# Performance work log

Hardware: AMD Instinct MI355X
Metric: run time of the kernel (lower is better)

Reference implementation:

```python
import jax, jax.numpy as jnp
import numpy as np

B = 262144
IN = 12
HID = 256
OUT = 12


def setup_inputs() -> dict:
    key = jax.random.key(0)
    ks = jax.random.split(key, 7)
    def lin(k, fan_in, fan_out):
        kw, kb = jax.random.split(k)
        bound = 1.0 / np.sqrt(fan_in)
        W = jax.random.uniform(kw, (fan_in, fan_out), jnp.float32, -bound, bound)
        b = jax.random.uniform(kb, (fan_out,), jnp.float32, -bound, bound)
        return W, b
    W1, b1 = lin(ks[0], IN, HID)
    W2, b2 = lin(ks[1], HID, HID)
    W3, b3 = lin(ks[2], HID, OUT)
    inp = jax.random.normal(ks[3], (B, IN), jnp.float32)
    return {"inp": inp, "W1": W1, "b1": b1, "W2": W2, "b2": b2, "W3": W3, "b3": b3}


def _forward(inp, W1, b1, W2, b2, W3, b3):
    h = jax.nn.relu(inp @ W1 + b1)
    h = jax.nn.relu(h @ W2 + b2)
    x = h @ W3 + b3  # [B, 12]

    pos = jnp.tanh(x[:, 0:3])
    vel = jnp.tanh(x[:, 3:6])
    pts = jax.nn.sigmoid(x[:, 6:7])
    clus = jnp.tanh(x[:, 7:10])
    sun = jnp.tanh(x[:, 10:12])

    # position clipped to unit sphere
    dist = jnp.linalg.norm(pos, axis=1, keepdims=True)  # [B,1]
    pos_c = jnp.where(dist > 1.0, pos / dist, pos)

    # inspected points: over-estimates set to 1, under-estimates set to previous
    prev = inp[:, 6:7]
    pts_c = jnp.where(pts > 1.0, 1.0, pts)
    pts_c = jnp.where(pts < prev, prev, pts_c)

    # cluster: push away from deputy if moving toward it, then clip to unit sphere
    delta = clus - inp[:, 7:10]
    deputy = inp[:, 0:3] - inp[:, 7:10]
    nd = deputy / jnp.linalg.norm(deputy, axis=1, keepdims=True)
    dd = jnp.einsum('ij,ij->i', delta, deputy)[:, None]  # [B,1]
    offset = jnp.where(dd > 0.0, clus - nd, clus)
    cdist = jnp.linalg.norm(offset, axis=1, keepdims=True)
    # NOTE: non-exceeding rows keep the ORIGINAL tanh prediction (torch semantics)
    clus_c = jnp.where(cdist > 1.0, offset / cdist, clus)

    # sun angle projected onto unit circle
    sun_c = sun / jnp.linalg.norm(sun, axis=1, keepdims=True)

    return jnp.concatenate([pos_c, vel, pts_c, clus_c, sun_c], axis=1)


def reference(inp, W1, b1, W2, b2, W3, b3):
    return _forward(inp, W1, b1, W2, b2, W3, b3)
```

## Files before the change

kernel.cpp:

```cpp
#include <hip/hip_runtime.h>
#include <math.h>

#define NIN 12
#define HID 256
#define NOUT 12
#define BM 64
#define NBLK (262144 / BM)

typedef _Float16 f16;
typedef f16 f16x8 __attribute__((ext_vector_type(8)));
typedef float f32x4 __attribute__((ext_vector_type(4)));

__device__ __forceinline__ void gll16(const void* g, void* l) {
    __builtin_amdgcn_global_load_lds(
        (const __attribute__((address_space(1))) unsigned int*)g,
        (__attribute__((address_space(3))) unsigned int*)l, 16, 0, 0);
}

__global__ void prep_w2(const float* __restrict__ W2, f16* __restrict__ w2p) {
    const int e = (blockIdx.x * 256 + threadIdx.x) * 4;
    const int k = e >> 8, col0 = e & 255;
    const float4 w = *(const float4*)(W2 + k * HID + col0);
    const int s = k >> 5, lgw = (k >> 3) & 3, j = k & 7;
    #pragma unroll
    for (int q = 0; q < 4; ++q) {
        const float v = ((const float*)&w)[q];
        const f16 hi = (f16)v;
        const f16 lo = (f16)(v - (float)hi);
        const int c = col0 + q, ct = c >> 4, cc = c & 15, l = (lgw << 4) | cc;
        w2p[(size_t)(((s*2 + 0)*16 + ct)*64 + l)*8 + j] = hi;
        w2p[(size_t)(((s*2 + 1)*16 + ct)*64 + l)*8 + j] = lo;
    }
}

__global__ __launch_bounds__(256, 3)
void mlp_main(const float* __restrict__ inp, const float* __restrict__ W1,
              const float* __restrict__ b1, const float* __restrict__ W2,
              const float* __restrict__ b2, const float* __restrict__ W3,
              const float* __restrict__ b3, const f16* __restrict__ w2p,
              float* __restrict__ out)
{
    __shared__ __align__(16) unsigned char smem[48896];
    __shared__ int nflag;
    __shared__ int flaglist[16];

    f16*   Bl   = (f16*)smem;
    float* W3s  = (float*)(smem + 32768);
    float* b2s  = (float*)(smem + 45056);
    float* h1f  = (float*)(smem + 46080);
    float* h2f  = (float*)(smem + 47104);
    float* psum = (float*)(smem + 48128);

    const int t    = threadIdx.x;
    const int lane = t & 63;
    const int wid  = t >> 6;
    const int cl   = lane & 15;
    const int lg   = lane >> 4;
    const int row0 = blockIdx.x * BM;

    if (t == 0) nflag = 0;

    {
        const char* w3c = (const char*)W3;
        #pragma unroll
        for (int i = 0; i < 3; ++i) {
            const int off = (wid*3 + i) * 1024;
            gll16(w3c + off + lane*16, (char*)W3s + off);
        }
        if (wid == 0) gll16((const char*)b2 + lane*16, (char*)b2s);
    }

    const int myrow = row0 + wid*16 + cl;
    float xin[12];
    {
        const f32x4* ip = (const f32x4*)(inp + (size_t)myrow * NIN);
        const f32x4 a = ip[0], b = ip[1], c = ip[2];
        xin[0]=a.x; xin[1]=a.y; xin[2]=a.z; xin[3]=a.w;
        xin[4]=b.x; xin[5]=b.y; xin[6]=b.z; xin[7]=b.w;
        xin[8]=c.x; xin[9]=c.y; xin[10]=c.z; xin[11]=c.w;
    }

    f32x4 acc[16];
    {
        const f32x4 zero = {0.f, 0.f, 0.f, 0.f};
        #pragma unroll
        for (int ct = 0; ct < 16; ++ct) acc[ct] = zero;
    }
    for (int s = 0; s < 8; ++s) {
        __syncthreads();
        const char* src = (const char*)w2p + (size_t)s * 32768;
        #pragma unroll
        for (int i = 0; i < 8; ++i) {
            const int off = (i*4 + wid) * 1024;
            gll16(src + off + lane*16, (char*)Bl + off);
        }
        const int k0 = 32*s + 8*lg;
        float a0[8];
        {
            const f32x4 bb0 = *(const f32x4*)(b1 + k0);
            const f32x4 bb1 = *(const f32x4*)(b1 + k0 + 4);
            a0[0]=bb0.x; a0[1]=bb0.y; a0[2]=bb0.z; a0[3]=bb0.w;
            a0[4]=bb1.x; a0[5]=bb1.y; a0[6]=bb1.z; a0[7]=bb1.w;
        }
        #pragma unroll
        for (int m = 0; m < 12; ++m) {
            const float xm = xin[m];
            const f32x4 w0 = *(const f32x4*)(W1 + m*HID + k0);
            const f32x4 w1 = *(const f32x4*)(W1 + m*HID + k0 + 4);
            a0[0] = fmaf(xm, w0.x, a0[0]); a0[1] = fmaf(xm, w0.y, a0[1]);
            a0[2] = fmaf(xm, w0.z, a0[2]); a0[3] = fmaf(xm, w0.w, a0[3]);
            a0[4] = fmaf(xm, w1.x, a0[4]); a0[5] = fmaf(xm, w1.y, a0[5]);
            a0[6] = fmaf(xm, w1.z, a0[6]); a0[7] = fmaf(xm, w1.w, a0[7]);
        }
        f16x8 ahi, alo;
        #pragma unroll
        for (int j = 0; j < 8; ++j) {
            const float h = fmaxf(a0[j], 0.f);
            const f16 hi = (f16)h;
            ahi[j] = hi;
            alo[j] = (f16)(h - (float)hi);
        }
        asm volatile("s_waitcnt vmcnt(0)" ::: "memory");
        __syncthreads();
        #pragma unroll
        for (int ct = 0; ct < 16; ++ct) {
            const f16x8 bhi = *(const f16x8*)((const char*)Bl + (size_t)(( 0 + ct)*64 + lane)*16);
            const f16x8 blo = *(const f16x8*)((const char*)Bl + (size_t)((16 + ct)*64 + lane)*16);
            acc[ct] = __builtin_amdgcn_mfma_f32_16x16x32_f16(ahi, bhi, acc[ct], 0, 0, 0);
            acc[ct] = __builtin_amdgcn_mfma_f32_16x16x32_f16(ahi, blo, acc[ct], 0, 0, 0);
            acc[ct] = __builtin_amdgcn_mfma_f32_16x16x32_f16(alo, bhi, acc[ct], 0, 0, 0);
        }
    }

    float x[12];
    {
        float part[4][8];
        #pragma unroll
        for (int q = 0; q < 4; ++q)
            #pragma unroll
            for (int jj = 0; jj < 8; ++jj) part[q][jj] = 0.f;

        #pragma unroll
        for (int ct = 0; ct < 16; ++ct) {
            const int col = ct*16 + cl;
            const float bv = b2s[col];
            const f32x4 w3a = *(const f32x4*)(W3s + col*12);
            const f32x4 w3b = *(const f32x4*)(W3s + col*12 + 4);
            #pragma unroll
            for (int q = 0; q < 4; ++q) {
                const float h2 = fmaxf(acc[ct][q] + bv, 0.f);
                part[q][0] = fmaf(h2, w3a.x, part[q][0]);
                part[q][1] = fmaf(h2, w3a.y, part[q][1]);
                part[q][2] = fmaf(h2, w3a.z, part[q][2]);
                part[q][3] = fmaf(h2, w3a.w, part[q][3]);
                part[q][4] = fmaf(h2, w3b.x, part[q][4]);
                part[q][5] = fmaf(h2, w3b.y, part[q][5]);
                part[q][6] = fmaf(h2, w3b.z, part[q][6]);
                part[q][7] = fmaf(h2, w3b.w, part[q][7]);
            }
        }
        #pragma unroll
        for (int m = 1; m < 16; m <<= 1) {
            #pragma unroll
            for (int q = 0; q < 4; ++q)
                #pragma unroll
                for (int jj = 0; jj < 8; ++jj)
                    part[q][jj] += __shfl_xor(part[q][jj], m);
        }
        if (cl < 4) {
            #pragma unroll
            for (int jj = 0; jj < 8; ++jj) x[jj] = part[cl][jj];
        }
    }
    {
        float part[4][4];
        #pragma unroll
        for (int q = 0; q < 4; ++q)
            #pragma unroll
            for (int jj = 0; jj < 4; ++jj) part[q][jj] = 0.f;

        #pragma unroll
        for (int ct = 0; ct < 16; ++ct) {
            const int col = ct*16 + cl;
            const float bv = b2s[col];
            const f32x4 w3c = *(const f32x4*)(W3s + col*12 + 8);
            #pragma unroll
            for (int q = 0; q < 4; ++q) {
                const float h2 = fmaxf(acc[ct][q] + bv, 0.f);
                part[q][0] = fmaf(h2, w3c.x, part[q][0]);
                part[q][1] = fmaf(h2, w3c.y, part[q][1]);
                part[q][2] = fmaf(h2, w3c.z, part[q][2]);
                part[q][3] = fmaf(h2, w3c.w, part[q][3]);
            }
        }
        #pragma unroll
        for (int m = 1; m < 16; m <<= 1) {
            #pragma unroll
            for (int q = 0; q < 4; ++q)
                #pragma unroll
                for (int jj = 0; jj < 4; ++jj)
                    part[q][jj] += __shfl_xor(part[q][jj], m);
        }
        if (cl < 4) {
            #pragma unroll
            for (int jj = 0; jj < 4; ++jj) x[8 + jj] = part[cl][jj];
        }
    }

    if (cl < 4) {
        const int R = wid*16 + 4*lg + cl;
        const int grow = row0 + R;
        #pragma unroll
        for (int jj = 0; jj < 12; ++jj) x[jj] += b3[jj];

        const f32x4* ip = (const f32x4*)(inp + (size_t)grow * NIN);
        const f32x4 iA = ip[0], iB = ip[1], iC = ip[2];
        const float in0=iA.x, in1=iA.y, in2=iA.z, in6=iB.z, in7=iB.w, in8=iC.x, in9=iC.y;

        const float pos0=tanhf(x[0]), pos1=tanhf(x[1]), pos2=tanhf(x[2]);
        const float vel0=tanhf(x[3]), vel1=tanhf(x[4]), vel2=tanhf(x[5]);
        const float pts = 1.f/(1.f+expf(-x[6]));
        const float cl0=tanhf(x[7]), cl1=tanhf(x[8]), cl2=tanhf(x[9]);
        const float sn0=tanhf(x[10]), sn1=tanhf(x[11]);

        const float dist = sqrtf(pos0*pos0 + pos1*pos1 + pos2*pos2);
        float pc0=pos0, pc1=pos1, pc2=pos2;
        if (dist > 1.0f) { pc0 = pos0/dist; pc1 = pos1/dist; pc2 = pos2/dist; }

        const float prev = in6;
        float pts_c = (pts > 1.0f) ? 1.0f : pts;
        pts_c = (pts < prev) ? prev : pts_c;

        const float de0 = cl0-in7, de1 = cl1-in8, de2 = cl2-in9;
        const float dp0 = in0-in7, dp1 = in1-in8, dp2 = in2-in9;
        const float dpn = sqrtf(dp0*dp0 + dp1*dp1 + dp2*dp2);
        const float nd0 = dp0/dpn, nd1 = dp1/dpn, nd2 = dp2/dpn;
        const float dd  = de0*dp0 + de1*dp1 + de2*dp2;
        float off0, off1, off2;
        if (dd > 0.0f) { off0 = cl0-nd0; off1 = cl1-nd1; off2 = cl2-nd2; }
        else           { off0 = cl0;     off1 = cl1;     off2 = cl2;     }
        const float cdist = sqrtf(off0*off0 + off1*off1 + off2*off2);
        float cc0, cc1, cc2;
        if (cdist > 1.0f) { cc0 = off0/cdist; cc1 = off1/cdist; cc2 = off2/cdist; }
        else              { cc0 = cl0;        cc1 = cl1;        cc2 = cl2;        }

        const float snn = sqrtf(sn0*sn0 + sn1*sn1);
        const float sc0 = sn0/snn, sc1 = sn1/snn;

        if (fabsf(dd) < 2e-4f || (dd > 0.f && fabsf(cdist - 1.f) < 2e-4f)) {
            const int slot = atomicAdd(&nflag, 1);
            if (slot < 16) flaglist[slot] = R;
        }

        f32x4* dst = (f32x4*)(out + (size_t)grow * NOUT);
        f32x4 o0 = {pc0, pc1, pc2, vel0};
        f32x4 o1 = {vel1, vel2, pts_c, cc0};
        f32x4 o2 = {cc1, cc2, sc0, sc1};
        dst[0] = o0; dst[1] = o1; dst[2] = o2;
    }
    __syncthreads();

    const int nf = (nflag < 16) ? nflag : 16;
    for (int f = 0; f < nf; ++f) {
        const int grow = row0 + flaglist[f];
        {
            float a = b1[t];
            const float* xr = inp + (size_t)grow * NIN;
            #pragma unroll
            for (int m = 0; m < 12; ++m) a = fmaf(xr[m], W1[m*HID + t], a);
            h1f[t] = fmaxf(a, 0.f);
        }
        __syncthreads();
        {
            float a = b2[t];
            for (int k = 0; k < HID; ++k) a = fmaf(h1f[k], W2[k*HID + t], a);
            h2f[t] = fmaxf(a, 0.f);
        }
        __syncthreads();
        if (t < 12*16) {
            const int jj = t >> 4, seg = t & 15;
            float a = 0.f;
            #pragma unroll
            for (int u = 0; u < 16; ++u) a = fmaf(h2f[seg*16 + u], W3[(seg*16 + u)*NOUT + jj], a);
            psum[jj*16 + seg] = a;
        }
        __syncthreads();
        if (t == 0) {
            float xx[12];
            #pragma unroll
            for (int jj = 0; jj < 12; ++jj) {
                float sacc = b3[jj];
                for (int g = 0; g < 16; ++g) sacc += psum[jj*16 + g];
                xx[jj] = sacc;
            }
            const float* xr = inp + (size_t)grow * NIN;
            const float in0=xr[0], in1=xr[1], in2=xr[2], in6=xr[6], in7=xr[7], in8=xr[8], in9=xr[9];
            const float pos0=tanhf(xx[0]), pos1=tanhf(xx[1]), pos2=tanhf(xx[2]);
            const float vel0=tanhf(xx[3]), vel1=tanhf(xx[4]), vel2=tanhf(xx[5]);
            const float pts = 1.f/(1.f+expf(-xx[6]));
            const float cl0=tanhf(xx[7]), cl1=tanhf(xx[8]), cl2=tanhf(xx[9]);
            const float sn0=tanhf(xx[10]), sn1=tanhf(xx[11]);
            const float dist = sqrtf(pos0*pos0 + pos1*pos1 + pos2*pos2);
            float pc0=pos0, pc1=pos1, pc2=pos2;
            if (dist > 1.0f) { pc0 = pos0/dist; pc1 = pos1/dist; pc2 = pos2/dist; }
            const float prev = in6;
            float pts_c = (pts > 1.0f) ? 1.0f : pts;
            pts_c = (pts < prev) ? prev : pts_c;
            const float de0 = cl0-in7, de1 = cl1-in8, de2 = cl2-in9;
            const float dp0 = in0-in7, dp1 = in1-in8, dp2 = in2-in9;
            const float dpn = sqrtf(dp0*dp0 + dp1*dp1 + dp2*dp2);
            const float nd0 = dp0/dpn, nd1 = dp1/dpn, nd2 = dp2/dpn;
            const float dd  = de0*dp0 + de1*dp1 + de2*dp2;
            float off0, off1, off2;
            if (dd > 0.0f) { off0 = cl0-nd0; off1 = cl1-nd1; off2 = cl2-nd2; }
            else           { off0 = cl0;     off1 = cl1;     off2 = cl2;     }
            const float cdist = sqrtf(off0*off0 + off1*off1 + off2*off2);
            float cc0, cc1, cc2;
            if (cdist > 1.0f) { cc0 = off0/cdist; cc1 = off1/cdist; cc2 = off2/cdist; }
            else              { cc0 = cl0;        cc1 = cl1;        cc2 = cl2;        }
            const float snn = sqrtf(sn0*sn0 + sn1*sn1);
            const float sc0 = sn0/snn, sc1 = sn1/snn;
            float* dst = out + (size_t)grow * NOUT;
            dst[0]=pc0; dst[1]=pc1; dst[2]=pc2; dst[3]=vel0; dst[4]=vel1; dst[5]=vel2;
            dst[6]=pts_c; dst[7]=cc0; dst[8]=cc1; dst[9]=cc2; dst[10]=sc0; dst[11]=sc1;
        }
        __syncthreads();
    }
}

extern "C" void kernel_launch(void* const* d_in, const int* in_sizes, int n_in,
                              void* d_out, int out_size, void* d_ws, size_t ws_size,
                              hipStream_t stream) {
    const float* inp = (const float*)d_in[0];
    const float* W1  = (const float*)d_in[1];
    const float* b1  = (const float*)d_in[2];
    const float* W2  = (const float*)d_in[3];
    const float* b2  = (const float*)d_in[4];
    const float* W3  = (const float*)d_in[5];
    const float* b3  = (const float*)d_in[6];
    float* out = (float*)d_out;
    f16* w2p = (f16*)d_ws;

    hipLaunchKernelGGL(prep_w2, dim3(64), dim3(256), 0, stream, W2, w2p);
    hipLaunchKernelGGL(mlp_main, dim3(NBLK), dim3(256), 0, stream,
                       inp, W1, b1, W2, b2, W3, b3, (const f16*)w2p, out);
}
```

Baseline: 254.0 us.

## Double-buffer W2 slabs and split output columns across 8 waves

Raises the block to 512 threads. The 8 waves split the 256 hidden output columns in two halves, so each wave holds 8 accumulators instead of 16. W2 slabs are double-buffered in LDS and the next slab is prefetched while MFMAs run on the current one, which removes the sync-load-wait bubble at every k step. W3 is loaded after the loop into the freed buffer, and partial outputs from the two column halves are reduced through LDS before the epilogue. In exchange, LDS per block grows to about 71 KB, the layer-1 ReLU work is duplicated across the column halves, and an extra reduction sync is added.

```diff
diff --git a/kernel.cpp b/kernel.cpp
--- a/kernel.cpp
+++ b/kernel.cpp
@@ -5,6 +5,7 @@
 #define HID 256
 #define NOUT 12
 #define BM 64
+#define THREADS 512
 #define NBLK (262144 / BM)
 
 typedef _Float16 f16;
@@ -33,44 +34,43 @@
     }
 }
 
-__global__ __launch_bounds__(256, 3)
+__global__ __launch_bounds__(THREADS, 4)
 void mlp_main(const float* __restrict__ inp, const float* __restrict__ W1,
               const float* __restrict__ b1, const float* __restrict__ W2,
               const float* __restrict__ b2, const float* __restrict__ W3,
               const float* __restrict__ b3, const f16* __restrict__ w2p,
               float* __restrict__ out)
 {
-    __shared__ __align__(16) unsigned char smem[48896];
+    __shared__ __align__(16) unsigned char smem[72704];
     __shared__ int nflag;
     __shared__ int flaglist[16];
 
-    f16*   Bl   = (f16*)smem;
-    float* W3s  = (float*)(smem + 32768);
-    float* b2s  = (float*)(smem + 45056);
-    float* h1f  = (float*)(smem + 46080);
-    float* h2f  = (float*)(smem + 47104);
-    float* psum = (float*)(smem + 48128);
+    float* b2s  = (float*)(smem + 65536);
+    float* psum = (float*)(smem + 66560);
+    float* W3s  = (float*)smem;
+    float* h1f  = (float*)(smem + 12288);
+    float* h2f  = (float*)(smem + 13312);
 
     const int t    = threadIdx.x;
     const int lane = t & 63;
     const int wid  = t >> 6;
+    const int wr   = wid & 3;
+    const int wc   = wid >> 2;
     const int cl   = lane & 15;
     const int lg   = lane >> 4;
     const int row0 = blockIdx.x * BM;
 
     if (t == 0) nflag = 0;
 
-    {
-        const char* w3c = (const char*)W3;
-        #pragma unroll
-        for (int i = 0; i < 3; ++i) {
-            const int off = (wid*3 + i) * 1024;
-            gll16(w3c + off + lane*16, (char*)W3s + off);
-        }
-        if (wid == 0) gll16((const char*)b2 + lane*16, (char*)b2s);
-    }
-
-    const int myrow = row0 + wid*16 + cl;
+    if (t < 64) gll16((const char*)b2 + t*16, smem + 65536 + t*16);
+    {
+        const char* src = (const char*)w2p;
+        #pragma unroll
+        for (int i = 0; i < 4; ++i)
+            gll16(src + (i*THREADS + t)*16, smem + (i*THREADS + t)*16);
+    }
+
+    const int myrow = row0 + wr*16 + cl;
     float xin[12];
     {
         const f32x4* ip = (const f32x4*)(inp + (size_t)myrow * NIN);
@@ -80,20 +80,14 @@
         xin[8]=c.x; xin[9]=c.y; xin[10]=c.z; xin[11]=c.w;
     }
 
-    f32x4 acc[16];
+    f32x4 acc[8];
     {
         const f32x4 zero = {0.f, 0.f, 0.f, 0.f};
         #pragma unroll
-        for (int ct = 0; ct < 16; ++ct) acc[ct] = zero;
-    }
+        for (int ct = 0; ct < 8; ++ct) acc[ct] = zero;
+    }
+    #pragma unroll
     for (int s = 0; s < 8; ++s) {
-        __syncthreads();
-        const char* src = (const char*)w2p + (size_t)s * 32768;
-        #pragma unroll
-        for (int i = 0; i < 8; ++i) {
-            const int off = (i*4 + wid) * 1024;
-            gll16(src + off + lane*16, (char*)Bl + off);
-        }
         const int k0 = 32*s + 8*lg;
         float a0[8];
         {
@@ -120,18 +114,39 @@
             ahi[j] = hi;
             alo[j] = (f16)(h - (float)hi);
         }
+
         asm volatile("s_waitcnt vmcnt(0)" ::: "memory");
         __syncthreads();
-        #pragma unroll
-        for (int ct = 0; ct < 16; ++ct) {
-            const f16x8 bhi = *(const f16x8*)((const char*)Bl + (size_t)(( 0 + ct)*64 + lane)*16);
-            const f16x8 blo = *(const f16x8*)((const char*)Bl + (size_t)((16 + ct)*64 + lane)*16);
+
+        if (s < 7) {
+            const char* src = (const char*)w2p + (size_t)(s+1) * 32768;
+            char* dst = (char*)smem + ((s+1)&1) * 32768;
+            #pragma unroll
+            for (int i = 0; i < 4; ++i)
+                gll16(src + (i*THREADS + t)*16, dst + (i*THREADS + t)*16);
+        }
+
+        const char* bufr = (const char*)smem + (s&1) * 32768;
+        #pragma unroll
+        for (int ct = 0; ct < 8; ++ct) {
+            const int gct = wc*8 + ct;
+            const f16x8 bhi = *(const f16x8*)(bufr + (size_t)(( 0 + gct)*64 + lane)*16);
+            const f16x8 blo = *(const f16x8*)(bufr + (size_t)((16 + gct)*64 + lane)*16);
             acc[ct] = __builtin_amdgcn_mfma_f32_16x16x32_f16(ahi, bhi, acc[ct], 0, 0, 0);
             acc[ct] = __builtin_amdgcn_mfma_f32_16x16x32_f16(ahi, blo, acc[ct], 0, 0, 0);
             acc[ct] = __builtin_amdgcn_mfma_f32_16x16x32_f16(alo, bhi, acc[ct], 0, 0, 0);
         }
     }
 
+    __syncthreads();
+    {
+        const char* w3c = (const char*)W3;
+        gll16(w3c + t*16, smem + t*16);
+        if (t < 256) gll16(w3c + 8192 + t*16, smem + 8192 + t*16);
+    }
+    asm volatile("s_waitcnt vmcnt(0)" ::: "memory");
+    __syncthreads();
+
     float x[12];
     {
         float part[4][8];
@@ -141,8 +156,8 @@
             for (int jj = 0; jj < 8; ++jj) part[q][jj] = 0.f;
 
         #pragma unroll
-        for (int ct = 0; ct < 16; ++ct) {
-            const int col = ct*16 + cl;
+        for (int ct = 0; ct < 8; ++ct) {
+            const int col = (wc*8 + ct)*16 + cl;
             const float bv = b2s[col];
             const f32x4 w3a = *(const f32x4*)(W3s + col*12);
             const f32x4 w3b = *(const f32x4*)(W3s + col*12 + 4);
@@ -160,13 +175,12 @@
             }
         }
         #pragma unroll
-        for (int m = 1; m < 16; m <<= 1) {
+        for (int m = 1; m < 16; m <<= 1)
             #pragma unroll
             for (int q = 0; q < 4; ++q)
                 #pragma unroll
                 for (int jj = 0; jj < 8; ++jj)
                     part[q][jj] += __shfl_xor(part[q][jj], m);
-        }
         if (cl < 4) {
             #pragma unroll
             for (int jj = 0; jj < 8; ++jj) x[jj] = part[cl][jj];
@@ -180,8 +194,8 @@
             for (int jj = 0; jj < 4; ++jj) part[q][jj] = 0.f;
 
         #pragma unroll
-        for (int ct = 0; ct < 16; ++ct) {
-            const int col = ct*16 + cl;
+        for (int ct = 0; ct < 8; ++ct) {
+            const int col = (wc*8 + ct)*16 + cl;
             const float bv = b2s[col];
             const f32x4 w3c = *(const f32x4*)(W3s + col*12 + 8);
             #pragma unroll
@@ -194,13 +208,12 @@
             }
         }
         #pragma unroll
-        for (int m = 1; m < 16; m <<= 1) {
+        for (int m = 1; m < 16; m <<= 1)
             #pragma unroll
             for (int q = 0; q < 4; ++q)
                 #pragma unroll
                 for (int jj = 0; jj < 4; ++jj)
                     part[q][jj] += __shfl_xor(part[q][jj], m);
-        }
         if (cl < 4) {
             #pragma unroll
             for (int jj = 0; jj < 4; ++jj) x[8 + jj] = part[cl][jj];
@@ -208,20 +221,30 @@
     }
 
     if (cl < 4) {
-        const int R = wid*16 + 4*lg + cl;
-        const int grow = row0 + R;
-        #pragma unroll
-        for (int jj = 0; jj < 12; ++jj) x[jj] += b3[jj];
+        const int R = wr*16 + 4*lg + cl;
+        float* p = psum + (size_t)(wc*BM + R) * 12;
+        #pragma unroll
+        for (int jj = 0; jj < 12; ++jj) p[jj] = x[jj];
+    }
+    __syncthreads();
+
+    if (t < BM) {
+        const int r = t;
+        const int grow = row0 + r;
+        float xr_[12];
+        #pragma unroll
+        for (int jj = 0; jj < 12; ++jj)
+            xr_[jj] = psum[r*12 + jj] + psum[(BM + r)*12 + jj] + b3[jj];
 
         const f32x4* ip = (const f32x4*)(inp + (size_t)grow * NIN);
         const f32x4 iA = ip[0], iB = ip[1], iC = ip[2];
         const float in0=iA.x, in1=iA.y, in2=iA.z, in6=iB.z, in7=iB.w, in8=iC.x, in9=iC.y;
 
-        const float pos0=tanhf(x[0]), pos1=tanhf(x[1]), pos2=tanhf(x[2]);
-        const float vel0=tanhf(x[3]), vel1=tanhf(x[4]), vel2=tanhf(x[5]);
-        const float pts = 1.f/(1.f+expf(-x[6]));
-        const float cl0=tanhf(x[7]), cl1=tanhf(x[8]), cl2=tanhf(x[9]);
-        const float sn0=tanhf(x[10]), sn1=tanhf(x[11]);
+        const float pos0=tanhf(xr_[0]), pos1=tanhf(xr_[1]), pos2=tanhf(xr_[2]);
+        const float vel0=tanhf(xr_[3]), vel1=tanhf(xr_[4]), vel2=tanhf(xr_[5]);
+        const float pts = 1.f/(1.f+expf(-xr_[6]));
+        const float cl0=tanhf(xr_[7]), cl1=tanhf(xr_[8]), cl2=tanhf(xr_[9]);
+        const float sn0=tanhf(xr_[10]), sn1=tanhf(xr_[11]);
 
         const float dist = sqrtf(pos0*pos0 + pos1*pos1 + pos2*pos2);
         float pc0=pos0, pc1=pos1, pc2=pos2;
@@ -249,7 +272,7 @@
 
         if (fabsf(dd) < 2e-4f || (dd > 0.f && fabsf(cdist - 1.f) < 2e-4f)) {
             const int slot = atomicAdd(&nflag, 1);
-            if (slot < 16) flaglist[slot] = R;
+            if (slot < 16) flaglist[slot] = r;
         }
 
         f32x4* dst = (f32x4*)(out + (size_t)grow * NOUT);
@@ -263,7 +286,7 @@
     const int nf = (nflag < 16) ? nflag : 16;
     for (int f = 0; f < nf; ++f) {
         const int grow = row0 + flaglist[f];
-        {
+        if (t < HID) {
             float a = b1[t];
             const float* xr = inp + (size_t)grow * NIN;
             #pragma unroll
@@ -271,7 +294,7 @@
             h1f[t] = fmaxf(a, 0.f);
         }
         __syncthreads();
-        {
+        if (t < HID) {
             float a = b2[t];
             for (int k = 0; k < HID; ++k) a = fmaf(h1f[k], W2[k*HID + t], a);
             h2f[t] = fmaxf(a, 0.f);
@@ -342,6 +365,6 @@
     f16* w2p = (f16*)d_ws;
 
     hipLaunchKernelGGL(prep_w2, dim3(64), dim3(256), 0, stream, W2, w2p);
-    hipLaunchKernelGGL(mlp_main, dim3(NBLK), dim3(256), 0, stream,
+    hipLaunchKernelGGL(mlp_main, dim3(NBLK), dim3(THREADS), 0, stream,
                        inp, W1, b1, W2, b2, W3, b3, (const f16*)w2p, out);
 }
```

Result: slower. 370.4 us (+45.8%).

## Use single fp16 MFMA for layer 2 with double-buffered W2 prefetch

Applied to the files above, without the earlier changes.

Drops the split hi/lo fp16 emulation of fp32 for the 256x256 layer, so each k-step issues one MFMA instead of three and the W2 tile halves in size. The W2 tiles are double-buffered in shared memory, with the next tile prefetched and the next layer-1 activations computed while the current MFMAs run. Launch bounds drop to two blocks per CU. To make up for the lower precision, the flag thresholds that send borderline rows to the exact fallback path are widened, which may send more rows down the slow path or miss rows that cross a branch boundary.

```diff
diff --git a/kernel.cpp b/kernel.cpp
--- a/kernel.cpp
+++ b/kernel.cpp
@@ -25,15 +25,12 @@
     #pragma unroll
     for (int q = 0; q < 4; ++q) {
         const float v = ((const float*)&w)[q];
-        const f16 hi = (f16)v;
-        const f16 lo = (f16)(v - (float)hi);
         const int c = col0 + q, ct = c >> 4, cc = c & 15, l = (lgw << 4) | cc;
-        w2p[(size_t)(((s*2 + 0)*16 + ct)*64 + l)*8 + j] = hi;
-        w2p[(size_t)(((s*2 + 1)*16 + ct)*64 + l)*8 + j] = lo;
+        w2p[(size_t)((s*16 + ct)*64 + l)*8 + j] = (f16)v;
     }
 }
 
-__global__ __launch_bounds__(256, 3)
+__global__ __launch_bounds__(256, 2)
 void mlp_main(const float* __restrict__ inp, const float* __restrict__ W1,
               const float* __restrict__ b1, const float* __restrict__ W2,
               const float* __restrict__ b2, const float* __restrict__ W3,
@@ -44,7 +41,6 @@
     __shared__ int nflag;
     __shared__ int flaglist[16];
 
-    f16*   Bl   = (f16*)smem;
     float* W3s  = (float*)(smem + 32768);
     float* b2s  = (float*)(smem + 45056);
     float* h1f  = (float*)(smem + 46080);
@@ -65,9 +61,12 @@
         #pragma unroll
         for (int i = 0; i < 3; ++i) {
             const int off = (wid*3 + i) * 1024;
-            gll16(w3c + off + lane*16, (char*)W3s + off);
-        }
-        if (wid == 0) gll16((const char*)b2 + lane*16, (char*)b2s);
+            gll16(w3c + off + lane*16, smem + 32768 + off);
+        }
+        if (wid == 0) gll16((const char*)b2 + lane*16, smem + 45056);
+        #pragma unroll
+        for (int i = 0; i < 4; ++i)
+            gll16((const char*)w2p + (i*256 + t)*16, smem + (i*256 + t)*16);
     }
 
     const int myrow = row0 + wid*16 + cl;
@@ -80,28 +79,14 @@
         xin[8]=c.x; xin[9]=c.y; xin[10]=c.z; xin[11]=c.w;
     }
 
-    f32x4 acc[16];
-    {
-        const f32x4 zero = {0.f, 0.f, 0.f, 0.f};
-        #pragma unroll
-        for (int ct = 0; ct < 16; ++ct) acc[ct] = zero;
-    }
-    for (int s = 0; s < 8; ++s) {
-        __syncthreads();
-        const char* src = (const char*)w2p + (size_t)s * 32768;
-        #pragma unroll
-        for (int i = 0; i < 8; ++i) {
-            const int off = (i*4 + wid) * 1024;
-            gll16(src + off + lane*16, (char*)Bl + off);
-        }
-        const int k0 = 32*s + 8*lg;
+    f16x8 aCur, aNxt;
+    {
+        const int k0 = 8*lg;
         float a0[8];
-        {
-            const f32x4 bb0 = *(const f32x4*)(b1 + k0);
-            const f32x4 bb1 = *(const f32x4*)(b1 + k0 + 4);
-            a0[0]=bb0.x; a0[1]=bb0.y; a0[2]=bb0.z; a0[3]=bb0.w;
-            a0[4]=bb1.x; a0[5]=bb1.y; a0[6]=bb1.z; a0[7]=bb1.w;
-        }
+        const f32x4 bb0 = *(const f32x4*)(b1 + k0);
+        const f32x4 bb1 = *(const f32x4*)(b1 + k0 + 4);
+        a0[0]=bb0.x; a0[1]=bb0.y; a0[2]=bb0.z; a0[3]=bb0.w;
+        a0[4]=bb1.x; a0[5]=bb1.y; a0[6]=bb1.z; a0[7]=bb1.w;
         #pragma unroll
         for (int m = 0; m < 12; ++m) {
             const float xm = xin[m];
@@ -112,24 +97,56 @@
             a0[4] = fmaf(xm, w1.x, a0[4]); a0[5] = fmaf(xm, w1.y, a0[5]);
             a0[6] = fmaf(xm, w1.z, a0[6]); a0[7] = fmaf(xm, w1.w, a0[7]);
         }
-        f16x8 ahi, alo;
-        #pragma unroll
-        for (int j = 0; j < 8; ++j) {
-            const float h = fmaxf(a0[j], 0.f);
-            const f16 hi = (f16)h;
-            ahi[j] = hi;
-            alo[j] = (f16)(h - (float)hi);
+        #pragma unroll
+        for (int j = 0; j < 8; ++j) aCur[j] = (f16)fmaxf(a0[j], 0.f);
+    }
+    asm volatile("s_waitcnt vmcnt(0)" ::: "memory");
+    __syncthreads();
+
+    f32x4 acc[16];
+    {
+        const f32x4 zero = {0.f, 0.f, 0.f, 0.f};
+        #pragma unroll
+        for (int ct = 0; ct < 16; ++ct) acc[ct] = zero;
+    }
+    #pragma unroll
+    for (int s = 0; s < 8; ++s) {
+        if (s < 7) {
+            const char* src = (const char*)w2p + (size_t)(s+1) * 16384;
+            char* dst = (char*)smem + ((s+1)&1) * 16384;
+            #pragma unroll
+            for (int i = 0; i < 4; ++i)
+                gll16(src + (i*256 + t)*16, dst + (i*256 + t)*16);
+        }
+        const char* bufr = (const char*)smem + (s&1) * 16384;
+        #pragma unroll
+        for (int ct = 0; ct < 16; ++ct) {
+            const f16x8 bfrag = *(const f16x8*)(bufr + (size_t)(ct*64 + lane)*16);
+            acc[ct] = __builtin_amdgcn_mfma_f32_16x16x32_f16(aCur, bfrag, acc[ct], 0, 0, 0);
+        }
+        if (s < 7) {
+            const int k0 = 32*(s+1) + 8*lg;
+            float a0[8];
+            const f32x4 bb0 = *(const f32x4*)(b1 + k0);
+            const f32x4 bb1 = *(const f32x4*)(b1 + k0 + 4);
+            a0[0]=bb0.x; a0[1]=bb0.y; a0[2]=bb0.z; a0[3]=bb0.w;
+            a0[4]=bb1.x; a0[5]=bb1.y; a0[6]=bb1.z; a0[7]=bb1.w;
+            #pragma unroll
+            for (int m = 0; m < 12; ++m) {
+                const float xm = xin[m];
+                const f32x4 w0 = *(const f32x4*)(W1 + m*HID + k0);
+                const f32x4 w1 = *(const f32x4*)(W1 + m*HID + k0 + 4);
+                a0[0] = fmaf(xm, w0.x, a0[0]); a0[1] = fmaf(xm, w0.y, a0[1]);
+                a0[2] = fmaf(xm, w0.z, a0[2]); a0[3] = fmaf(xm, w0.w, a0[3]);
+                a0[4] = fmaf(xm, w1.x, a0[4]); a0[5] = fmaf(xm, w1.y, a0[5]);
+                a0[6] = fmaf(xm, w1.z, a0[6]); a0[7] = fmaf(xm, w1.w, a0[7]);
+            }
+            #pragma unroll
+            for (int j = 0; j < 8; ++j) aNxt[j] = (f16)fmaxf(a0[j], 0.f);
         }
         asm volatile("s_waitcnt vmcnt(0)" ::: "memory");
         __syncthreads();
-        #pragma unroll
-        for (int ct = 0; ct < 16; ++ct) {
-            const f16x8 bhi = *(const f16x8*)((const char*)Bl + (size_t)(( 0 + ct)*64 + lane)*16);
-            const f16x8 blo = *(const f16x8*)((const char*)Bl + (size_t)((16 + ct)*64 + lane)*16);
-            acc[ct] = __builtin_amdgcn_mfma_f32_16x16x32_f16(ahi, bhi, acc[ct], 0, 0, 0);
-            acc[ct] = __builtin_amdgcn_mfma_f32_16x16x32_f16(ahi, blo, acc[ct], 0, 0, 0);
-            acc[ct] = __builtin_amdgcn_mfma_f32_16x16x32_f16(alo, bhi, acc[ct], 0, 0, 0);
-        }
+        if (s < 7) aCur = aNxt;
     }
 
     float x[12];
@@ -160,13 +177,12 @@
             }
         }
         #pragma unroll
-        for (int m = 1; m < 16; m <<= 1) {
+        for (int m = 1; m < 16; m <<= 1)
             #pragma unroll
             for (int q = 0; q < 4; ++q)
                 #pragma unroll
                 for (int jj = 0; jj < 8; ++jj)
                     part[q][jj] += __shfl_xor(part[q][jj], m);
-        }
         if (cl < 4) {
             #pragma unroll
             for (int jj = 0; jj < 8; ++jj) x[jj] = part[cl][jj];
@@ -194,13 +210,12 @@
             }
         }
         #pragma unroll
-        for (int m = 1; m < 16; m <<= 1) {
+        for (int m = 1; m < 16; m <<= 1)
             #pragma unroll
             for (int q = 0; q < 4; ++q)
                 #pragma unroll
                 for (int jj = 0; jj < 4; ++jj)
                     part[q][jj] += __shfl_xor(part[q][jj], m);
-        }
         if (cl < 4) {
             #pragma unroll
             for (int jj = 0; jj < 4; ++jj) x[8 + jj] = part[cl][jj];
@@ -247,7 +262,7 @@
         const float snn = sqrtf(sn0*sn0 + sn1*sn1);
         const float sc0 = sn0/snn, sc1 = sn1/snn;
 
-        if (fabsf(dd) < 2e-4f || (dd > 0.f && fabsf(cdist - 1.f) < 2e-4f)) {
+        if (fabsf(dd) < 8e-3f || (dd > 0.f && fabsf(cdist - 1.f) < 4e-3f)) {
             const int slot = atomicAdd(&nflag, 1);
             if (slot < 16) flaglist[slot] = R;
         }
```

After: 287.5 us. 1.13x slower.

## Double-buffer W2 slabs in LDS to overlap loads with MFMA

Applied to the files above, without the earlier changes.

Replaces the single 32KB W2 staging buffer with two ping-pong buffers, prefetching the next K-slab through global_load_lds while the current slab feeds the MFMAs. It waits on a partial vmcnt instead of draining all loads. W3 loading is deferred until after the main loop so its LDS region can be reused. LDS use per block grows to about 69KB and launch bounds drop from 3 to 2 blocks per CU, trading occupancy for overlap.

```diff
diff --git a/kernel.cpp b/kernel.cpp
--- a/kernel.cpp
+++ b/kernel.cpp
@@ -33,23 +33,22 @@
     }
 }
 
-__global__ __launch_bounds__(256, 3)
+__global__ __launch_bounds__(256, 2)
 void mlp_main(const float* __restrict__ inp, const float* __restrict__ W1,
               const float* __restrict__ b1, const float* __restrict__ W2,
               const float* __restrict__ b2, const float* __restrict__ W3,
               const float* __restrict__ b3, const f16* __restrict__ w2p,
               float* __restrict__ out)
 {
-    __shared__ __align__(16) unsigned char smem[48896];
+    __shared__ __align__(16) unsigned char smem[69376];
     __shared__ int nflag;
     __shared__ int flaglist[16];
 
-    f16*   Bl   = (f16*)smem;
-    float* W3s  = (float*)(smem + 32768);
-    float* b2s  = (float*)(smem + 45056);
-    float* h1f  = (float*)(smem + 46080);
-    float* h2f  = (float*)(smem + 47104);
-    float* psum = (float*)(smem + 48128);
+    float* W3s  = (float*)smem;
+    float* b2s  = (float*)(smem + 65536);
+    float* h1f  = (float*)(smem + 66560);
+    float* h2f  = (float*)(smem + 67584);
+    float* psum = (float*)(smem + 68608);
 
     const int t    = threadIdx.x;
     const int lane = t & 63;
@@ -61,13 +60,12 @@
     if (t == 0) nflag = 0;
 
     {
-        const char* w3c = (const char*)W3;
-        #pragma unroll
-        for (int i = 0; i < 3; ++i) {
-            const int off = (wid*3 + i) * 1024;
-            gll16(w3c + off + lane*16, (char*)W3s + off);
-        }
-        if (wid == 0) gll16((const char*)b2 + lane*16, (char*)b2s);
+        if (wid == 0) gll16((const char*)b2 + lane*16, smem + 65536);
+        #pragma unroll
+        for (int i = 0; i < 8; ++i) {
+            const int off = (i*4 + wid) * 1024;
+            gll16((const char*)w2p + off + lane*16, smem + off);
+        }
     }
 
     const int myrow = row0 + wid*16 + cl;
@@ -86,13 +84,16 @@
         #pragma unroll
         for (int ct = 0; ct < 16; ++ct) acc[ct] = zero;
     }
+    #pragma unroll
     for (int s = 0; s < 8; ++s) {
-        __syncthreads();
-        const char* src = (const char*)w2p + (size_t)s * 32768;
-        #pragma unroll
-        for (int i = 0; i < 8; ++i) {
-            const int off = (i*4 + wid) * 1024;
-            gll16(src + off + lane*16, (char*)Bl + off);
+        if (s < 7) {
+            const char* src = (const char*)w2p + (size_t)(s+1) * 32768;
+            char* dst = (char*)smem + ((s+1)&1) * 32768;
+            #pragma unroll
+            for (int i = 0; i < 8; ++i) {
+                const int off = (i*4 + wid) * 1024;
+                gll16(src + off + lane*16, dst + off);
+            }
         }
         const int k0 = 32*s + 8*lg;
         float a0[8];
@@ -120,17 +121,32 @@
             ahi[j] = hi;
             alo[j] = (f16)(h - (float)hi);
         }
-        asm volatile("s_waitcnt vmcnt(0)" ::: "memory");
-        __syncthreads();
+        if (s < 7) { asm volatile("s_waitcnt vmcnt(8)" ::: "memory"); }
+        else       { asm volatile("s_waitcnt vmcnt(0)" ::: "memory"); }
+        __syncthreads();
+
+        const char* bufr = (const char*)smem + (s&1) * 32768;
         #pragma unroll
         for (int ct = 0; ct < 16; ++ct) {
-            const f16x8 bhi = *(const f16x8*)((const char*)Bl + (size_t)(( 0 + ct)*64 + lane)*16);
-            const f16x8 blo = *(const f16x8*)((const char*)Bl + (size_t)((16 + ct)*64 + lane)*16);
+            const f16x8 bhi = *(const f16x8*)(bufr + (size_t)(( 0 + ct)*64 + lane)*16);
+            const f16x8 blo = *(const f16x8*)(bufr + (size_t)((16 + ct)*64 + lane)*16);
             acc[ct] = __builtin_amdgcn_mfma_f32_16x16x32_f16(ahi, bhi, acc[ct], 0, 0, 0);
             acc[ct] = __builtin_amdgcn_mfma_f32_16x16x32_f16(ahi, blo, acc[ct], 0, 0, 0);
             acc[ct] = __builtin_amdgcn_mfma_f32_16x16x32_f16(alo, bhi, acc[ct], 0, 0, 0);
         }
-    }
+        __syncthreads();
+    }
+
+    {
+        const char* w3c = (const char*)W3;
+        #pragma unroll
+        for (int i = 0; i < 3; ++i) {
+            const int off = (wid*3 + i) * 1024;
+            gll16(w3c + off + lane*16, smem + off);
+        }
+    }
+    asm volatile("s_waitcnt vmcnt(0)" ::: "memory");
+    __syncthreads();
 
     float x[12];
     {
@@ -160,13 +176,12 @@
             }
         }
         #pragma unroll
-        for (int m = 1; m < 16; m <<= 1) {
+        for (int m = 1; m < 16; m <<= 1)
             #pragma unroll
             for (int q = 0; q < 4; ++q)
                 #pragma unroll
                 for (int jj = 0; jj < 8; ++jj)
                     part[q][jj] += __shfl_xor(part[q][jj], m);
-        }
         if (cl < 4) {
             #pragma unroll
             for (int jj = 0; jj < 8; ++jj) x[jj] = part[cl][jj];
@@ -194,13 +209,12 @@
             }
         }
         #pragma unroll
-        for (int m = 1; m < 16; m <<= 1) {
+        for (int m = 1; m < 16; m <<= 1)
             #pragma unroll
             for (int q = 0; q < 4; ++q)
                 #pragma unroll
                 for (int jj = 0; jj < 4; ++jj)
                     part[q][jj] += __shfl_xor(part[q][jj], m);
-        }
         if (cl < 4) {
             #pragma unroll
             for (int jj = 0; jj < 4; ++jj) x[8 + jj] = part[cl][jj];
```

New measurement: 236.6 us. 1.07x faster.
